# Kernel optimization log

Hardware: AMD Instinct MI355X
Metric: run time of the kernel (lower is better)

Reference implementation:

```python
import jax, jax.numpy as jnp
import numpy as np

N = 50000      # nodes
E = 800000     # edges (avg degree 16)
F_IN = 512
HID = 128
OUT = 40


def setup_inputs() -> dict:
    key = jax.random.key(0)
    ks = jax.random.split(key, 6)
    x = jax.random.normal(ks[0], (N, F_IN), dtype=jnp.float32)
    edge_index = jax.random.randint(ks[1], (2, E), 0, N, dtype=jnp.int64)
    edge_weight = jax.random.uniform(ks[2], (E,), dtype=jnp.float32)
    # Glorot-ish init for the two GCNConv weight matrices
    W1 = jax.random.normal(ks[3], (F_IN, HID), dtype=jnp.float32) * (1.0 / np.sqrt(F_IN))
    b1 = jnp.zeros((HID,), dtype=jnp.float32)
    W2 = jax.random.normal(ks[4], (HID, OUT), dtype=jnp.float32) * (1.0 / np.sqrt(HID))
    b2 = jnp.zeros((OUT,), dtype=jnp.float32)
    return {"x": x, "edge_index": edge_index, "edge_weight": edge_weight,
            "W1": W1, "b1": b1, "W2": W2, "b2": b2}


def gcn_layer(x, edge_index, edge_weight, W, b):
    """PyG GCNConv (normalize=True, add_self_loops=True):
    out = D^{-1/2} (A + I) D^{-1/2} (x @ W) + b, with weighted edges."""
    n = x.shape[0]
    h = x @ W  # [n, F_out] dense transform before aggregation
    sl = jnp.arange(n)
    row = jnp.concatenate([edge_index[0], sl])   # source nodes
    col = jnp.concatenate([edge_index[1], sl])   # target nodes
    w = jnp.concatenate([edge_weight, jnp.ones((n,), x.dtype)])  # self-loop weight 1
    deg = jax.ops.segment_sum(w, col, num_segments=n)            # in-degree (weighted)
    dinv = jnp.where(deg > 0, jax.lax.rsqrt(deg), 0.0)
    norm = dinv[row] * w * dinv[col]                             # per-edge coefficient
    # gather-source, scale, scatter-add into target
    out = jax.ops.segment_sum(h[row] * norm[:, None], col, num_segments=n)
    return out + b


def reference(x, edge_index, edge_weight, W1, b1, W2, b2):
    h = jax.nn.relu(gcn_layer(x, edge_index, edge_weight, W1, b1))
    # dropout is identity at inference (training=False)
    h = gcn_layer(h, edge_index, edge_weight, W2, b2)
    return jax.nn.log_softmax(h, axis=1)
```

## Files before the change

### kernel.cpp

```cpp
#include <hip/hip_runtime.h>
#include <math.h>

#define N_NODES 50000
#define F_IN    512
#define HID     128
#define OUT_C   40
#define NPAD    48
#define E_EDGES 800000
#define LDA 40
#define LDK 136
#define MAXDEG 64
#define ESTRIDE 40
#define G1B 391
#define DEGB 3125

typedef __attribute__((ext_vector_type(8))) short short8;
typedef __attribute__((ext_vector_type(4))) float f32x4;
typedef __attribute__((ext_vector_type(4))) unsigned uint4v;

__device__ __forceinline__ unsigned short f2bf(float f) {
    union { float f; unsigned u; } v; v.f = f;
    unsigned u = v.u + 0x7fffu + ((v.u >> 16) & 1u);
    return (unsigned short)(u >> 16);
}
__device__ __forceinline__ float bflo(unsigned u) { return __uint_as_float(u << 16); }
__device__ __forceinline__ float bfhi(unsigned u) { return __uint_as_float(u & 0xffff0000u); }
__device__ __forceinline__ unsigned cvtpk(float lo, float hi) {
    unsigned r;
    asm("v_cvt_pk_bf16_f32 %0, %1, %2" : "=v"(r) : "v"(lo), "v"(hi));
    return r;
}
__device__ __forceinline__ float pk2dinv(unsigned pk) {
    return rsqrtf(1.0f + (float)(pk & 0x03FFFFFFu) * (1.0f / 1048576.0f));
}


__global__ __launch_bounds__(256) void k_initwprep(const float* __restrict__ W1,
                                                   const float* __restrict__ W2,
                                                   unsigned short* __restrict__ W1bt,
                                                   unsigned short* __restrict__ W2bt,
                                                   unsigned* __restrict__ packed) {
    int idx = blockIdx.x * 256 + threadIdx.x;
    if (idx < N_NODES) packed[idx] = 0u;
    if (idx < F_IN * HID) {
        int k = idx & 511, n = idx >> 9;
        W1bt[(size_t)n * F_IN + k] = f2bf(W1[(size_t)k * HID + n]);
    } else if (idx < F_IN * HID + NPAD * HID) {
        int i2 = idx - F_IN * HID;
        int k = i2 & 127, n = i2 >> 7;
        W2bt[n * HID + k] = (n < OUT_C) ? f2bf(W2[(size_t)k * OUT_C + n]) : 0;
    }
}


__global__ __launch_bounds__(256) void k_g1deg(const float* __restrict__ X,
                                               const unsigned short* __restrict__ W1bt,
                                               unsigned short* __restrict__ Hb,
                                               const int* __restrict__ row,
                                               const int* __restrict__ col,
                                               const float* __restrict__ ew,
                                               unsigned* __restrict__ packed,
                                               unsigned* __restrict__ es) {
    const int tid = threadIdx.x;
    if (blockIdx.x >= G1B) {
        int e = (blockIdx.x - G1B) * 256 + tid;
        if (e < E_EDGES) {
            int c   = col[e];
            int r   = row[e];
            float w = ew[e];
            unsigned fx = (unsigned)(w * 1048576.0f);
            unsigned old = atomicAdd(&packed[c], (1u << 26) | fx);
            int rk = (int)(old >> 26);
            if (rk < ESTRIDE)
                es[(size_t)c * ESTRIDE + rk] = (unsigned)r | ((unsigned)f2bf(w) << 16);
        }
        return;
    }

    __shared__ __align__(16) unsigned short As[128 * LDA];
    __shared__ __align__(16) unsigned short Bs[128 * LDA];
    const int row0 = blockIdx.x * 128;
    const int lane = tid & 63;
    const int w    = tid >> 6;
    const int quad = lane >> 4;
    const int l16  = lane & 15;
    const int wm   = (w >> 1) * 64;
    const int wn   = (w & 1) * 64;

    f32x4 acc[4][4] = {};

    const int sr = tid >> 1;
    const int kg = (tid & 1) * 16;
    int arow = row0 + sr;
    if (arow >= N_NODES) arow = N_NODES - 1;
    const float*          xp = X + (size_t)arow * F_IN + kg;
    const unsigned short* bp = W1bt + (size_t)sr * F_IN + kg;
    unsigned short* asw = &As[sr * LDA + kg];
    unsigned short* bsw = &Bs[sr * LDA + kg];

    float4 xa = *(const float4*)(xp);
    float4 xb = *(const float4*)(xp + 4);
    float4 xc = *(const float4*)(xp + 8);
    float4 xd = *(const float4*)(xp + 12);
    short8 wa = *(const short8*)(bp);
    short8 wb = *(const short8*)(bp + 8);

    for (int k0 = 0; k0 < F_IN; k0 += 32) {
        uint4v pa, pb;
        pa[0] = cvtpk(xa.x, xa.y); pa[1] = cvtpk(xa.z, xa.w);
        pa[2] = cvtpk(xb.x, xb.y); pa[3] = cvtpk(xb.z, xb.w);
        pb[0] = cvtpk(xc.x, xc.y); pb[1] = cvtpk(xc.z, xc.w);
        pb[2] = cvtpk(xd.x, xd.y); pb[3] = cvtpk(xd.z, xd.w);
        short8 cwa = wa, cwb = wb;

        if (k0 + 32 < F_IN) {
            xa = *(const float4*)(xp + k0 + 32);
            xb = *(const float4*)(xp + k0 + 36);
            xc = *(const float4*)(xp + k0 + 40);
            xd = *(const float4*)(xp + k0 + 44);
            wa = *(const short8*)(bp + k0 + 32);
            wb = *(const short8*)(bp + k0 + 40);
        }

        *(uint4v*)(asw)      = pa;
        *(uint4v*)(asw + 8)  = pb;
        *(short8*)(bsw)      = cwa;
        *(short8*)(bsw + 8)  = cwb;
        asm volatile("s_waitcnt lgkmcnt(0)" ::: "memory");
        __builtin_amdgcn_s_barrier();
        asm volatile("" ::: "memory");

        short8 af[4], bf[4];
#pragma unroll
        for (int i = 0; i < 4; i++)
            af[i] = *(const short8*)&As[(wm + i * 16 + l16) * LDA + quad * 8];
#pragma unroll
        for (int j = 0; j < 4; j++)
            bf[j] = *(const short8*)&Bs[(wn + j * 16 + l16) * LDA + quad * 8];
#pragma unroll
        for (int i = 0; i < 4; i++)
#pragma unroll
            for (int j = 0; j < 4; j++)
                acc[i][j] = __builtin_amdgcn_mfma_f32_16x16x32_bf16(
                    af[i], bf[j], acc[i][j], 0, 0, 0);
        asm volatile("" ::: "memory");
        __builtin_amdgcn_s_barrier();
        asm volatile("" ::: "memory");
    }

#pragma unroll
    for (int i = 0; i < 4; i++) {
#pragma unroll
        for (int r = 0; r < 4; r++) {
            int grow = row0 + wm + i * 16 + quad * 4 + r;
            if (grow < N_NODES) {
#pragma unroll
                for (int j = 0; j < 4; j++) {
                    int gcol = wn + j * 16 + l16;
                    Hb[(size_t)grow * HID + gcol] = f2bf(acc[i][j][r]);
                }
            }
        }
    }
}


__global__ __launch_bounds__(256) void k_agg1(const unsigned* __restrict__ packed,
                                              const unsigned* __restrict__ es,
                                              const unsigned short* __restrict__ H1b,
                                              const float* __restrict__ b1,
                                              unsigned short* __restrict__ A1b) {
    __shared__ int2 sE[4][MAXDEG];
    const int tid  = threadIdx.x;
    const int wv   = tid >> 6;
    const int lane = tid & 63;
    const int node = blockIdx.x * 4 + wv;
    if (node >= N_NODES) return;
    const int q   = lane >> 4;
    const int l16 = lane & 15;

    const unsigned pkn = packed[node];
    const int   d  = (int)(pkn >> 26);
    const float di = pk2dinv(pkn);
    const size_t base = (size_t)node * ESTRIDE;
    int dl = (d < ESTRIDE) ? d : ESTRIDE;
    const int dp = (dl + 15) & ~15;
    for (int p = lane; p < dp; p += 64) {
        int2 t = make_int2(0, 0);
        if (p < dl) {
            unsigned u = es[base + p];
            float dv = pk2dinv(packed[u & 0xffffu]);
            t.x = (int)(u & 0xffffu);
            t.y = __float_as_int(bfhi(u) * dv);
        }
        sE[wv][p] = t;
    }

    const uint4 sv = *(const uint4*)&H1b[(size_t)node * HID + l16 * 8];
    float a[8];
    if (q == 0) {
        a[0] = di * bflo(sv.x); a[1] = di * bfhi(sv.x);
        a[2] = di * bflo(sv.y); a[3] = di * bfhi(sv.y);
        a[4] = di * bflo(sv.z); a[5] = di * bfhi(sv.z);
        a[6] = di * bflo(sv.w); a[7] = di * bfhi(sv.w);
    } else {
#pragma unroll
        for (int k = 0; k < 8; k++) a[k] = 0.0f;
    }

    for (int p = 0; p < dp; p += 16) {
        const int bs = p + q * 4;
        int s_[4]; float n_[4];
#pragma unroll
        for (int j = 0; j < 4; j++) {
            int2 t = sE[wv][bs + j];
            s_[j] = t.x; n_[j] = __int_as_float(t.y);
        }
        uint4 g[4];
#pragma unroll
        for (int j = 0; j < 4; j++)
            g[j] = *(const uint4*)&H1b[(size_t)s_[j] * HID + l16 * 8];
#pragma unroll
        for (int j = 0; j < 4; j++) {
            a[0] = fmaf(bflo(g[j].x), n_[j], a[0]);
            a[1] = fmaf(bfhi(g[j].x), n_[j], a[1]);
            a[2] = fmaf(bflo(g[j].y), n_[j], a[2]);
            a[3] = fmaf(bfhi(g[j].y), n_[j], a[3]);
            a[4] = fmaf(bflo(g[j].z), n_[j], a[4]);
            a[5] = fmaf(bfhi(g[j].z), n_[j], a[5]);
            a[6] = fmaf(bflo(g[j].w), n_[j], a[6]);
            a[7] = fmaf(bfhi(g[j].w), n_[j], a[7]);
        }
    }

#pragma unroll
    for (int k = 0; k < 8; k++) {
        a[k] += __shfl_xor(a[k], 16);
        a[k] += __shfl_xor(a[k], 32);
    }

    if (q == 0) {
        const float4 bv0 = *(const float4*)&b1[l16 * 8];
        const float4 bv1 = *(const float4*)&b1[l16 * 8 + 4];
        float r0 = fmaxf(fmaf(di, a[0], bv0.x), 0.0f);
        float r1 = fmaxf(fmaf(di, a[1], bv0.y), 0.0f);
        float r2 = fmaxf(fmaf(di, a[2], bv0.z), 0.0f);
        float r3 = fmaxf(fmaf(di, a[3], bv0.w), 0.0f);
        float r4 = fmaxf(fmaf(di, a[4], bv1.x), 0.0f);
        float r5 = fmaxf(fmaf(di, a[5], bv1.y), 0.0f);
        float r6 = fmaxf(fmaf(di, a[6], bv1.z), 0.0f);
        float r7 = fmaxf(fmaf(di, a[7], bv1.w), 0.0f);
        uint4 pk4;
        pk4.x = cvtpk(r0, r1);
        pk4.y = cvtpk(r2, r3);
        pk4.z = cvtpk(r4, r5);
        pk4.w = cvtpk(r6, r7);
        *(uint4*)&A1b[(size_t)node * HID + l16 * 8] = pk4;
    }
}


__global__ __launch_bounds__(256) void k_gemm2_mfma(const unsigned short* __restrict__ A1b,
                                                    const unsigned short* __restrict__ W2bt,
                                                    const unsigned* __restrict__ packed,
                                                    unsigned short* __restrict__ H2b) {
    __shared__ __align__(16) unsigned short As[128 * LDK];
    __shared__ __align__(16) unsigned short Bs[NPAD * LDK];
    const int tid  = threadIdx.x;
    const int row0 = blockIdx.x * 128;
    const int lane = tid & 63;
    const int w    = tid >> 6;
    const int quad = lane >> 4;
    const int l16  = lane & 15;

#pragma unroll
    for (int i = 0; i < 8; i++) {
        int id = tid + i * 256;
        int r = id >> 4, kc = (id & 15) * 8;
        int ar = row0 + r; if (ar >= N_NODES) ar = N_NODES - 1;
        *(short8*)&As[r * LDK + kc] = *(const short8*)&A1b[(size_t)ar * HID + kc];
    }
#pragma unroll
    for (int i = 0; i < 3; i++) {
        int id = tid + i * 256;
        int n = id >> 4, kc = (id & 15) * 8;
        *(short8*)&Bs[n * LDK + kc] = *(const short8*)&W2bt[n * HID + kc];
    }
    __syncthreads();

    f32x4 acc[2][3] = {};
    const int rbase = w * 32;
#pragma unroll
    for (int ks = 0; ks < 4; ks++) {
        const int k0 = ks * 32 + quad * 8;
        short8 af[2], bf[3];
#pragma unroll
        for (int i = 0; i < 2; i++)
            af[i] = *(const short8*)&As[(rbase + i * 16 + l16) * LDK + k0];
#pragma unroll
        for (int j = 0; j < 3; j++)
            bf[j] = *(const short8*)&Bs[(j * 16 + l16) * LDK + k0];
#pragma unroll
        for (int i = 0; i < 2; i++)
#pragma unroll
            for (int j = 0; j < 3; j++)
                acc[i][j] = __builtin_amdgcn_mfma_f32_16x16x32_bf16(
                    af[i], bf[j], acc[i][j], 0, 0, 0);
    }

#pragma unroll
    for (int i = 0; i < 2; i++) {
#pragma unroll
        for (int r = 0; r < 4; r++) {
            int grow = row0 + rbase + i * 16 + quad * 4 + r;
            if (grow < N_NODES) {
                float dv = pk2dinv(packed[grow]);
#pragma unroll
                for (int j = 0; j < 3; j++)
                    H2b[(size_t)grow * NPAD + j * 16 + l16] = f2bf(dv * acc[i][j][r]);
            }
        }
    }
}


__global__ __launch_bounds__(256) void k_agg2_lsm(const unsigned* __restrict__ packed,
                                                  const unsigned* __restrict__ es,
                                                  const unsigned short* __restrict__ H2b,
                                                  const float* __restrict__ b2,
                                                  float* __restrict__ out) {
    __shared__ int2 sE[4][MAXDEG];
    const int tid  = threadIdx.x;
    const int wv   = tid >> 6;
    const int lane = tid & 63;
    const int node = blockIdx.x * 4 + wv;
    if (node >= N_NODES) return;
    const int h = lane >> 5;
    const int l = lane & 31;
    const bool act = (l < 20);

    const unsigned pkn = packed[node];
    const int   d  = (int)(pkn >> 26);
    const float di = pk2dinv(pkn);
    const size_t base = (size_t)node * ESTRIDE;
    int dl = (d < ESTRIDE) ? d : ESTRIDE;
    const int dp = (dl + 15) & ~15;
    for (int p = lane; p < dp; p += 64) {
        int2 t = make_int2(0, 0);
        if (p < dl) {
            unsigned u = es[base + p];
            t.x = (int)(u & 0xffffu);
            t.y = __float_as_int(bfhi(u));
        }
        sE[wv][p] = t;
    }

    float a0 = 0.0f, a1 = 0.0f;
    if (h == 0 && act) {
        unsigned sv = *(const unsigned*)&H2b[(size_t)node * NPAD + 2 * l];
        a0 = bflo(sv); a1 = bfhi(sv);
    }

    for (int p = 0; p < dp; p += 16) {
        const int bs = p + h * 8;
        int s_[8]; float n_[8];
#pragma unroll
        for (int j = 0; j < 8; j++) {
            int2 t = sE[wv][bs + j];
            s_[j] = t.x; n_[j] = __int_as_float(t.y);
        }
        if (act) {
            unsigned g[8];
#pragma unroll
            for (int j = 0; j < 8; j++)
                g[j] = *(const unsigned*)&H2b[(size_t)s_[j] * NPAD + 2 * l];
#pragma unroll
            for (int j = 0; j < 8; j++) {
                a0 = fmaf(bflo(g[j]), n_[j], a0);
                a1 = fmaf(bfhi(g[j]), n_[j], a1);
            }
        }
    }

    a0 += __shfl_xor(a0, 32);
    a1 += __shfl_xor(a1, 32);

    float v0 = 0.0f, v1 = 0.0f;
    if (act) {
        float2 bv = *(const float2*)&b2[2 * l];
        v0 = fmaf(di, a0, bv.x);
        v1 = fmaf(di, a1, bv.y);
    }

    float m = act ? fmaxf(v0, v1) : -INFINITY;
#pragma unroll
    for (int off = 16; off > 0; off >>= 1) m = fmaxf(m, __shfl_xor(m, off));
    float ex = act ? (__expf(v0 - m) + __expf(v1 - m)) : 0.0f;
    float s = ex;
#pragma unroll
    for (int off = 16; off > 0; off >>= 1) s += __shfl_xor(s, off);
    if (h == 0 && act) {
        float lg = __logf(s);
        *(float2*)&out[(size_t)node * OUT_C + 2 * l] =
            make_float2(v0 - m - lg, v1 - m - lg);
    }
}


extern "C" void kernel_launch(void* const* d_in, const int* in_sizes, int n_in,
                              void* d_out, int out_size, void* d_ws, size_t ws_size,
                              hipStream_t stream) {
    const float* x  = (const float*)d_in[0];
    const int*   ei = (const int*)d_in[1];
    const float* ew = (const float*)d_in[2];
    const float* W1 = (const float*)d_in[3];
    const float* b1 = (const float*)d_in[4];
    const float* W2 = (const float*)d_in[5];
    const float* b2 = (const float*)d_in[6];
    float* out = (float*)d_out;

    const int* row = ei;
    const int* col = ei + E_EDGES;

    float* ws = (float*)d_ws;
    unsigned* packed     = (unsigned*)ws;
    unsigned short* H1b  = (unsigned short*)(ws + 100000);
    unsigned short* H2b  = (unsigned short*)(ws + 100000);
    unsigned short* A1b  = (unsigned short*)(ws + 3300000);
    unsigned short* W1bt = (unsigned short*)(ws + 6500000);
    unsigned short* W2bt = (unsigned short*)(ws + 6532768);
    unsigned* es         = (unsigned*)(ws + 6535840);

    const int B = 256;

    k_initwprep<<<(F_IN * HID + NPAD * HID + B - 1) / B, B, 0, stream>>>(
        W1, W2, W1bt, W2bt, packed);

    k_g1deg<<<G1B + DEGB, B, 0, stream>>>(x, W1bt, H1b, row, col, ew, packed, es);

    k_agg1<<<(N_NODES + 3) / 4, B, 0, stream>>>(packed, es, H1b, b1, A1b);

    k_gemm2_mfma<<<(N_NODES + 127) / 128, B, 0, stream>>>(A1b, W2bt, packed, H2b);

    k_agg2_lsm<<<(N_NODES + 3) / 4, B, 0, stream>>>(packed, es, H2b, b2, out);
}
```

Before: 257.1 us.

## Pack per-node degree and first neighbors into one 64-byte record; widen agg2 lanes

Each node's degree counter and its first 15 neighbor entries now sit together in a single 16-word record, with later neighbors spilled to an overflow array. Aggregation can then read the degree and most of the edge list from one cache line instead of two separate arrays. The layer-2 aggregation also changes from 2 to 4 features per lane, so each wave handles 4 neighbors in parallel instead of 2. The cost is a larger zero-init region, which grows the init grid, and atomics spread 64 bytes apart, which may hurt locality for the dinv lookups of neighbor nodes.

Measured after the change: 272.8 us. 1.06x slower.

```diff
diff --git a/kernel.cpp b/kernel.cpp
--- a/kernel.cpp
+++ b/kernel.cpp
@@ -11,6 +11,9 @@
 #define LDK 136
 #define MAXDEG 64
 #define ESTRIDE 40
+#define NBW 16
+#define INLINE_SLOTS 15
+#define OV 25
 #define G1B 391
 #define DEGB 3125
 
@@ -39,9 +42,9 @@
                                                    const float* __restrict__ W2,
                                                    unsigned short* __restrict__ W1bt,
                                                    unsigned short* __restrict__ W2bt,
-                                                   unsigned* __restrict__ packed) {
+                                                   unsigned* __restrict__ nb) {
     int idx = blockIdx.x * 256 + threadIdx.x;
-    if (idx < N_NODES) packed[idx] = 0u;
+    if (idx < N_NODES * NBW) nb[idx] = 0u;
     if (idx < F_IN * HID) {
         int k = idx & 511, n = idx >> 9;
         W1bt[(size_t)n * F_IN + k] = f2bf(W1[(size_t)k * HID + n]);
@@ -59,8 +62,8 @@
                                                const int* __restrict__ row,
                                                const int* __restrict__ col,
                                                const float* __restrict__ ew,
-                                               unsigned* __restrict__ packed,
-                                               unsigned* __restrict__ es) {
+                                               unsigned* __restrict__ nb,
+                                               unsigned* __restrict__ es2) {
     const int tid = threadIdx.x;
     if (blockIdx.x >= G1B) {
         int e = (blockIdx.x - G1B) * 256 + tid;
@@ -69,10 +72,13 @@
             int r   = row[e];
             float w = ew[e];
             unsigned fx = (unsigned)(w * 1048576.0f);
-            unsigned old = atomicAdd(&packed[c], (1u << 26) | fx);
+            unsigned old = atomicAdd(&nb[(size_t)c * NBW], (1u << 26) | fx);
             int rk = (int)(old >> 26);
-            if (rk < ESTRIDE)
-                es[(size_t)c * ESTRIDE + rk] = (unsigned)r | ((unsigned)f2bf(w) << 16);
+            unsigned ent = (unsigned)r | ((unsigned)f2bf(w) << 16);
+            if (rk < INLINE_SLOTS)
+                nb[(size_t)c * NBW + 1 + rk] = ent;
+            else if (rk < ESTRIDE)
+                es2[(size_t)c * OV + (rk - INLINE_SLOTS)] = ent;
         }
         return;
     }
@@ -165,8 +171,8 @@
 }
 
 
-__global__ __launch_bounds__(256) void k_agg1(const unsigned* __restrict__ packed,
-                                              const unsigned* __restrict__ es,
+__global__ __launch_bounds__(256) void k_agg1(const unsigned* __restrict__ nb,
+                                              const unsigned* __restrict__ es2,
                                               const unsigned short* __restrict__ H1b,
                                               const float* __restrict__ b1,
                                               unsigned short* __restrict__ A1b) {
@@ -179,17 +185,18 @@
     const int q   = lane >> 4;
     const int l16 = lane & 15;
 
-    const unsigned pkn = packed[node];
+    const unsigned pkn = nb[(size_t)node * NBW];
     const int   d  = (int)(pkn >> 26);
     const float di = pk2dinv(pkn);
-    const size_t base = (size_t)node * ESTRIDE;
     int dl = (d < ESTRIDE) ? d : ESTRIDE;
     const int dp = (dl + 15) & ~15;
     for (int p = lane; p < dp; p += 64) {
         int2 t = make_int2(0, 0);
         if (p < dl) {
-            unsigned u = es[base + p];
-            float dv = pk2dinv(packed[u & 0xffffu]);
+            unsigned u = (p < INLINE_SLOTS)
+                       ? nb[(size_t)node * NBW + 1 + p]
+                       : es2[(size_t)node * OV + (p - INLINE_SLOTS)];
+            float dv = pk2dinv(nb[(size_t)(u & 0xffffu) * NBW]);
             t.x = (int)(u & 0xffffu);
             t.y = __float_as_int(bfhi(u) * dv);
         }
@@ -262,7 +269,7 @@
 
 __global__ __launch_bounds__(256) void k_gemm2_mfma(const unsigned short* __restrict__ A1b,
                                                     const unsigned short* __restrict__ W2bt,
-                                                    const unsigned* __restrict__ packed,
+                                                    const unsigned* __restrict__ nb,
                                                     unsigned short* __restrict__ H2b) {
     __shared__ __align__(16) unsigned short As[128 * LDK];
     __shared__ __align__(16) unsigned short Bs[NPAD * LDK];
@@ -314,7 +321,7 @@
         for (int r = 0; r < 4; r++) {
             int grow = row0 + rbase + i * 16 + quad * 4 + r;
             if (grow < N_NODES) {
-                float dv = pk2dinv(packed[grow]);
+                float dv = pk2dinv(nb[(size_t)grow * NBW]);
 #pragma unroll
                 for (int j = 0; j < 3; j++)
                     H2b[(size_t)grow * NPAD + j * 16 + l16] = f2bf(dv * acc[i][j][r]);
@@ -324,8 +331,8 @@
 }
 
 
-__global__ __launch_bounds__(256) void k_agg2_lsm(const unsigned* __restrict__ packed,
-                                                  const unsigned* __restrict__ es,
+__global__ __launch_bounds__(256) void k_agg2_lsm(const unsigned* __restrict__ nb,
+                                                  const unsigned* __restrict__ es2,
                                                   const unsigned short* __restrict__ H2b,
                                                   const float* __restrict__ b2,
                                                   float* __restrict__ out) {
@@ -335,74 +342,87 @@
     const int lane = tid & 63;
     const int node = blockIdx.x * 4 + wv;
     if (node >= N_NODES) return;
-    const int h = lane >> 5;
-    const int l = lane & 31;
-    const bool act = (l < 20);
-
-    const unsigned pkn = packed[node];
+    const int q   = lane >> 4;
+    const int l16 = lane & 15;
+    const bool act = (l16 < 10);
+
+    const unsigned pkn = nb[(size_t)node * NBW];
     const int   d  = (int)(pkn >> 26);
     const float di = pk2dinv(pkn);
-    const size_t base = (size_t)node * ESTRIDE;
     int dl = (d < ESTRIDE) ? d : ESTRIDE;
     const int dp = (dl + 15) & ~15;
     for (int p = lane; p < dp; p += 64) {
         int2 t = make_int2(0, 0);
         if (p < dl) {
-            unsigned u = es[base + p];
+            unsigned u = (p < INLINE_SLOTS)
+                       ? nb[(size_t)node * NBW + 1 + p]
+                       : es2[(size_t)node * OV + (p - INLINE_SLOTS)];
             t.x = (int)(u & 0xffffu);
             t.y = __float_as_int(bfhi(u));
         }
         sE[wv][p] = t;
     }
 
-    float a0 = 0.0f, a1 = 0.0f;
-    if (h == 0 && act) {
-        unsigned sv = *(const unsigned*)&H2b[(size_t)node * NPAD + 2 * l];
-        a0 = bflo(sv); a1 = bfhi(sv);
+    float a[4] = {0.0f, 0.0f, 0.0f, 0.0f};
+    if (q == 0 && act) {
+        uint2 sv = *(const uint2*)&H2b[(size_t)node * NPAD + 4 * l16];
+        a[0] = bflo(sv.x); a[1] = bfhi(sv.x);
+        a[2] = bflo(sv.y); a[3] = bfhi(sv.y);
     }
 
     for (int p = 0; p < dp; p += 16) {
-        const int bs = p + h * 8;
-        int s_[8]; float n_[8];
-#pragma unroll
-        for (int j = 0; j < 8; j++) {
+        const int bs = p + q * 4;
+        int s_[4]; float n_[4];
+#pragma unroll
+        for (int j = 0; j < 4; j++) {
             int2 t = sE[wv][bs + j];
             s_[j] = t.x; n_[j] = __int_as_float(t.y);
         }
         if (act) {
-            unsigned g[8];
-#pragma unroll
-            for (int j = 0; j < 8; j++)
-                g[j] = *(const unsigned*)&H2b[(size_t)s_[j] * NPAD + 2 * l];
-#pragma unroll
-            for (int j = 0; j < 8; j++) {
-                a0 = fmaf(bflo(g[j]), n_[j], a0);
-                a1 = fmaf(bfhi(g[j]), n_[j], a1);
+            uint2 g[4];
+#pragma unroll
+            for (int j = 0; j < 4; j++)
+                g[j] = *(const uint2*)&H2b[(size_t)s_[j] * NPAD + 4 * l16];
+#pragma unroll
+            for (int j = 0; j < 4; j++) {
+                a[0] = fmaf(bflo(g[j].x), n_[j], a[0]);
+                a[1] = fmaf(bfhi(g[j].x), n_[j], a[1]);
+                a[2] = fmaf(bflo(g[j].y), n_[j], a[2]);
+                a[3] = fmaf(bfhi(g[j].y), n_[j], a[3]);
             }
         }
     }
 
-    a0 += __shfl_xor(a0, 32);
-    a1 += __shfl_xor(a1, 32);
-
-    float v0 = 0.0f, v1 = 0.0f;
+#pragma unroll
+    for (int k = 0; k < 4; k++) {
+        a[k] += __shfl_xor(a[k], 16);
+        a[k] += __shfl_xor(a[k], 32);
+    }
+
+    float v[4];
+    float m = -INFINITY;
     if (act) {
-        float2 bv = *(const float2*)&b2[2 * l];
-        v0 = fmaf(di, a0, bv.x);
-        v1 = fmaf(di, a1, bv.y);
-    }
-
-    float m = act ? fmaxf(v0, v1) : -INFINITY;
-#pragma unroll
-    for (int off = 16; off > 0; off >>= 1) m = fmaxf(m, __shfl_xor(m, off));
-    float ex = act ? (__expf(v0 - m) + __expf(v1 - m)) : 0.0f;
+        const float4 bv = *(const float4*)&b2[4 * l16];
+        v[0] = fmaf(di, a[0], bv.x);
+        v[1] = fmaf(di, a[1], bv.y);
+        v[2] = fmaf(di, a[2], bv.z);
+        v[3] = fmaf(di, a[3], bv.w);
+        m = fmaxf(fmaxf(v[0], v[1]), fmaxf(v[2], v[3]));
+    }
+#pragma unroll
+    for (int off = 8; off > 0; off >>= 1) m = fmaxf(m, __shfl_xor(m, off));
+    float ex = 0.0f;
+    if (act)
+        ex = __expf(v[0] - m) + __expf(v[1] - m) + __expf(v[2] - m) + __expf(v[3] - m);
     float s = ex;
 #pragma unroll
-    for (int off = 16; off > 0; off >>= 1) s += __shfl_xor(s, off);
-    if (h == 0 && act) {
+    for (int off = 8; off > 0; off >>= 1) s += __shfl_xor(s, off);
+    if (q == 0 && act) {
         float lg = __logf(s);
-        *(float2*)&out[(size_t)node * OUT_C + 2 * l] =
-            make_float2(v0 - m - lg, v1 - m - lg);
+        float4 o;
+        o.x = v[0] - m - lg; o.y = v[1] - m - lg;
+        o.z = v[2] - m - lg; o.w = v[3] - m - lg;
+        *(float4*)&out[(size_t)node * OUT_C + 4 * l16] = o;
     }
 }
 
@@ -423,24 +443,24 @@
     const int* col = ei + E_EDGES;
 
     float* ws = (float*)d_ws;
-    unsigned* packed     = (unsigned*)ws;
-    unsigned short* H1b  = (unsigned short*)(ws + 100000);
-    unsigned short* H2b  = (unsigned short*)(ws + 100000);
-    unsigned short* A1b  = (unsigned short*)(ws + 3300000);
-    unsigned short* W1bt = (unsigned short*)(ws + 6500000);
-    unsigned short* W2bt = (unsigned short*)(ws + 6532768);
-    unsigned* es         = (unsigned*)(ws + 6535840);
+    unsigned* nb         = (unsigned*)ws;
+    unsigned short* H1b  = (unsigned short*)(ws + 800000);
+    unsigned short* H2b  = (unsigned short*)(ws + 800000);
+    unsigned short* A1b  = (unsigned short*)(ws + 4000000);
+    unsigned short* W1bt = (unsigned short*)(ws + 7200000);
+    unsigned short* W2bt = (unsigned short*)(ws + 7232768);
+    unsigned* es2        = (unsigned*)(ws + 7235840);
 
     const int B = 256;
 
-    k_initwprep<<<(F_IN * HID + NPAD * HID + B - 1) / B, B, 0, stream>>>(
-        W1, W2, W1bt, W2bt, packed);
-
-    k_g1deg<<<G1B + DEGB, B, 0, stream>>>(x, W1bt, H1b, row, col, ew, packed, es);
-
-    k_agg1<<<(N_NODES + 3) / 4, B, 0, stream>>>(packed, es, H1b, b1, A1b);
-
-    k_gemm2_mfma<<<(N_NODES + 127) / 128, B, 0, stream>>>(A1b, W2bt, packed, H2b);
-
-    k_agg2_lsm<<<(N_NODES + 3) / 4, B, 0, stream>>>(packed, es, H2b, b2, out);
-}
+    k_initwprep<<<(N_NODES * NBW + B - 1) / B, B, 0, stream>>>(
+        W1, W2, W1bt, W2bt, nb);
+
+    k_g1deg<<<G1B + DEGB, B, 0, stream>>>(x, W1bt, H1b, row, col, ew, nb, es2);
+
+    k_agg1<<<(N_NODES + 3) / 4, B, 0, stream>>>(nb, es2, H1b, b1, A1b);
+
+    k_gemm2_mfma<<<(N_NODES + 127) / 128, B, 0, stream>>>(A1b, W2bt, nb, H2b);
+
+    k_agg2_lsm<<<(N_NODES + 3) / 4, B, 0, stream>>>(nb, es2, H2b, b2, out);
+}
```
